# Kernel optimization log

Measured on AMD Instinct MI355X. Metric: run time of the kernel, lower is better.

The kernel has to match this reference:

```python
import jax, jax.numpy as jnp
import numpy as np

B, T, C = 2, 2048, 2048
H, HKV, D = 16, 4, 128
GROUPS = H // HKV  # num_key_value_groups
EPS = 1e-6


def setup_inputs() -> dict:
    key = jax.random.key(0)
    ks = jax.random.split(key, 6)
    s = 0.02
    return {
        "hidden_states": jax.random.normal(ks[0], (B, T, C), jnp.float32),
        "Wq": jax.random.normal(ks[1], (C, H * D), jnp.float32) * s,
        "Wk": jax.random.normal(ks[2], (C, HKV * D), jnp.float32) * s,
        "Wv": jax.random.normal(ks[3], (C, HKV * D), jnp.float32) * s,
        "Wo": jax.random.normal(ks[4], (H * D, C), jnp.float32) * s,
        "keep_mask": jax.random.randint(ks[5], (T,), 0, 2) > 0,
    }


def reference(hidden_states, Wq, Wk, Wv, Wo, keep_mask):
    # Base attention (standard causal GQA attention with output_attentions=True)
    q = (hidden_states @ Wq).reshape(B, T, H, D).transpose(0, 2, 1, 3)      # [B,H,T,D]
    k = (hidden_states @ Wk).reshape(B, T, HKV, D).transpose(0, 2, 1, 3)    # [B,Hkv,S,D]
    v = (hidden_states @ Wv).reshape(B, T, HKV, D).transpose(0, 2, 1, 3)    # [B,Hkv,S,D]
    k_rep = jnp.repeat(k, GROUPS, axis=1)                                    # [B,H,S,D]
    v_rep = jnp.repeat(v, GROUPS, axis=1)                                    # [B,H,S,D]
    scale = 1.0 / jnp.sqrt(jnp.float32(D))
    scores = jnp.einsum("bhtd,bhsd->bhts", q, k_rep) * scale                 # [B,H,T,S]
    causal = jnp.tril(jnp.ones((T, T), dtype=bool))
    scores = jnp.where(causal[None, None], scores, jnp.float32(-1e9))
    attn_w = jax.nn.softmax(scores, axis=-1)                                 # [B,H,T,S]

    # ScratchpadPrunedAttention: mask dropped positions, renormalize,
    # recompute context and o_proj.
    keep = keep_mask.astype(attn_w.dtype)[None, None, None, :]               # [1,1,1,S]
    attn_w = attn_w * keep
    attn_w = attn_w / (attn_w.sum(-1, keepdims=True) + EPS)
    new_ctx = jnp.einsum("bhts,bhsd->bhtd", attn_w, v_rep)                   # [B,H,T,D]
    new_ctx = new_ctx.transpose(0, 2, 1, 3).reshape(B, T, H * D)             # [B,T,H*D]
    out = new_ctx @ Wo                                                        # [B,T,C]
    return out, attn_w
```

## Files before the change

kernel.cpp:

```cpp
#include <hip/hip_runtime.h>
#include <hip/hip_bf16.h>
#include <stdint.h>

#define B_ 2
#define T_ 2048
#define C_ 2048
#define H_ 16
#define HKV_ 4
#define D_ 128
#define M_ (B_*T_)
static constexpr float SCL = 0.08838834764831845f * 1.4426950408889634f;
static constexpr float EPS_ = 1e-6f;

typedef short bf16x8 __attribute__((ext_vector_type(8)));
typedef float f32x4 __attribute__((ext_vector_type(4)));

__device__ __forceinline__ f32x4 zero4() {
  f32x4 v; v[0] = 0.f; v[1] = 0.f; v[2] = 0.f; v[3] = 0.f; return v;
}

__device__ __forceinline__ unsigned short f2bf(float x) {
  union { float f; unsigned u; } v; v.f = x;
  unsigned r = (v.u + 0x7FFFu + ((v.u >> 16) & 1u)) >> 16;
  return (unsigned short)r;
}

__device__ __forceinline__ void gl_lds16(const void* g, void* l) {
  __builtin_amdgcn_global_load_lds((const __attribute__((address_space(1))) void*)g,
                                   (__attribute__((address_space(3))) void*)l, 16, 0, 0);
}

__global__ void k_cvt(const float* __restrict__ in, unsigned short* __restrict__ out, int n) {
  int i = (blockIdx.x * blockDim.x + threadIdx.x) * 8;
  int stride = gridDim.x * blockDim.x * 8;
  for (; i < n; i += stride) {
    float4 a = *(const float4*)(in + i);
    float4 b = *(const float4*)(in + i + 4);
    ushort4 o0; o0.x = f2bf(a.x); o0.y = f2bf(a.y); o0.z = f2bf(a.z); o0.w = f2bf(a.w);
    ushort4 o1; o1.x = f2bf(b.x); o1.y = f2bf(b.y); o1.z = f2bf(b.z); o1.w = f2bf(b.w);
    *(ushort4*)(out + i) = o0;
    *(ushort4*)(out + i + 4) = o1;
  }
}

__global__ void k_cvt_t(const float* __restrict__ in, unsigned short* __restrict__ out,
                        int R, int Cc) {
  __shared__ float ld[32][33];
  int c0 = blockIdx.x * 32, r0 = blockIdx.y * 32;
  int x = threadIdx.x, y = threadIdx.y;
#pragma unroll
  for (int i = 0; i < 4; i++)
    ld[y * 4 + i][x] = in[(size_t)(r0 + y * 4 + i) * Cc + c0 + x];
  __syncthreads();
#pragma unroll
  for (int i = 0; i < 4; i++)
    out[(size_t)(c0 + y * 4 + i) * R + r0 + x] = f2bf(ld[x][y * 4 + i]);
}

template <int WRITE_F32>
__global__ __launch_bounds__(256) void k_gemm(const unsigned short* __restrict__ A,
                                              const unsigned short* __restrict__ Bt,
                                              void* __restrict__ Cout,
                                              int Mdim, int Ndim, int K) {
  __shared__ __align__(16) unsigned short As[128 * 64];
  __shared__ __align__(16) unsigned short Bs[128 * 64];
  const int tid = threadIdx.x;
  const int wid = tid >> 6, lane = tid & 63;
  const int wm = wid >> 1, wn = wid & 1;
  const int m0 = blockIdx.y * 128, n0 = blockIdx.x * 128;
  const int lrow = tid >> 3, lcol = (tid & 7) * 8;
  const int g = lane >> 4, lr = lane & 15;

  f32x4 acc[4][4];
#pragma unroll
  for (int i = 0; i < 4; i++)
#pragma unroll
    for (int j = 0; j < 4; j++) acc[i][j] = zero4();

  for (int k0 = 0; k0 < K; k0 += 64) {
    __syncthreads();
#pragma unroll
    for (int it = 0; it < 4; it++) {
      gl_lds16(A + (size_t)(m0 + lrow + it * 32) * K + k0 + lcol, (void*)(As + tid * 8 + it * 2048));
      gl_lds16(Bt + (size_t)(n0 + lrow + it * 32) * K + k0 + lcol, (void*)(Bs + tid * 8 + it * 2048));
    }
    __syncthreads();
#pragma unroll
    for (int kk = 0; kk < 2; kk++) {
      bf16x8 af[4], bfr[4];
#pragma unroll
      for (int i = 0; i < 4; i++)
        af[i] = *(const bf16x8*)(As + (wm * 64 + i * 16 + lr) * 64 + kk * 32 + g * 8);
#pragma unroll
      for (int j = 0; j < 4; j++)
        bfr[j] = *(const bf16x8*)(Bs + (wn * 64 + j * 16 + lr) * 64 + kk * 32 + g * 8);
#pragma unroll
      for (int i = 0; i < 4; i++)
#pragma unroll
        for (int j = 0; j < 4; j++)
          acc[i][j] = __builtin_amdgcn_mfma_f32_16x16x32_bf16(af[i], bfr[j], acc[i][j], 0, 0, 0);
    }
  }

#pragma unroll
  for (int i = 0; i < 4; i++)
#pragma unroll
    for (int j = 0; j < 4; j++)
#pragma unroll
      for (int r = 0; r < 4; r++) {
        int row = m0 + wm * 64 + i * 16 + g * 4 + r;
        int col = n0 + wn * 64 + j * 16 + lr;
        if (WRITE_F32)
          ((float*)Cout)[(size_t)row * Ndim + col] = acc[i][j][r];
        else
          ((unsigned short*)Cout)[(size_t)row * Ndim + col] = f2bf(acc[i][j][r]);
      }
}

__global__ __launch_bounds__(256) void k_attn(const unsigned short* __restrict__ qb,
                                              const unsigned short* __restrict__ kb,
                                              const unsigned short* __restrict__ vt,
                                              const int* __restrict__ mask,
                                              float* __restrict__ attn,
                                              unsigned short* __restrict__ ctx)
{
  __shared__ __align__(16) unsigned short Ks[64 * 128];
  __shared__ __align__(16) unsigned short Vs[128 * 64];
  __shared__ __align__(16) unsigned short Ps[4][16 * 64];
  __shared__ float keeps[2048];

  const int tid = threadIdx.x;
  const int wid = tid >> 6, lane = tid & 63;
  const int g = lane >> 4, lr = lane & 15;
  const int lr7 = lr & 7;
  const int qt = 31 - blockIdx.y;
  const int bh = blockIdx.x;
  const int b = bh >> 4, h = bh & 15, hkv = h >> 2;
  const int qbase = qt * 64;

  const unsigned short* qp = qb + (size_t)(b * T_ + qbase) * 2048 + h * 128;
  const unsigned short* kp = kb + (size_t)(b * T_) * 512 + hkv * 128;
  const unsigned short* vp = vt + (size_t)(hkv * 128) * 4096 + b * T_;
  float* ap = attn + (size_t)(bh * T_ + qbase) * 2048;
  unsigned short* cp = ctx + (size_t)(b * T_ + qbase) * 2048 + h * 128;

#pragma unroll
  for (int i = 0; i < 8; i++)
    keeps[tid * 8 + i] = (mask[tid * 8 + i] != 0) ? 1.0f : 0.0f;

  bf16x8 qa[4];
#pragma unroll
  for (int ks = 0; ks < 4; ks++)
    qa[ks] = *(const bf16x8*)(qp + (size_t)(wid * 16 + lr) * 2048 + ks * 32 + g * 8);

  const int ntile = qt + 1;
  float z[4] = {0, 0, 0, 0}, zk[4] = {0, 0, 0, 0};

  const int srow = tid >> 4;
  const int scolb = ((tid & 15) * 16) ^ ((srow & 7) << 4);
  const int vrow = tid >> 3;
  const int vcolb = ((tid & 7) * 16) ^ ((vrow & 7) << 4);

  for (int st = 0; st < ntile; st++) {
    int s0 = st * 64;
    __syncthreads();
#pragma unroll
    for (int it = 0; it < 4; it++)
      gl_lds16(kp + (size_t)(s0 + srow + it * 16) * 512 + (scolb >> 1),
               (void*)(Ks + tid * 8 + it * 2048));
    __syncthreads();
#pragma unroll
    for (int j = 0; j < 4; j++) {
      f32x4 sc = zero4();
      const unsigned short* kbase = Ks + (j * 16 + lr) * 128;
#pragma unroll
      for (int ks = 0; ks < 4; ks++) {
        bf16x8 kf = *(const bf16x8*)(kbase + (((ks * 64 + g * 16) ^ (lr7 << 4)) >> 1));
        sc = __builtin_amdgcn_mfma_f32_16x16x32_bf16(qa[ks], kf, sc, 0, 0, 0);
      }
      int sg = s0 + j * 16 + lr;
      float kpv = keeps[sg];
#pragma unroll
      for (int r = 0; r < 4; r++) {
        int tg = qbase + wid * 16 + g * 4 + r;
        float e = (sg <= tg) ? __builtin_amdgcn_exp2f(sc[r] * SCL) : 0.0f;
        z[r] += e;
        zk[r] += e * kpv;
      }
    }
  }
#pragma unroll
  for (int r = 0; r < 4; r++) {
#pragma unroll
    for (int m = 1; m < 16; m <<= 1) {
      z[r] += __shfl_xor(z[r], m);
      zk[r] += __shfl_xor(zk[r], m);
    }
  }
  float inv[4];
#pragma unroll
  for (int r = 0; r < 4; r++) inv[r] = 1.0f / (zk[r] + EPS_ * z[r]);

  f32x4 cacc[8];
#pragma unroll
  for (int n = 0; n < 8; n++) cacc[n] = zero4();

  for (int st = 0; st < 32; st++) {
    int s0 = st * 64;
    if (s0 > qbase + 63) {
      float4 zf; zf.x = 0.f; zf.y = 0.f; zf.z = 0.f; zf.w = 0.f;
#pragma unroll
      for (int it = 0; it < 4; it++) {
        int row = (tid >> 4) + it * 16;
        *(float4*)(ap + (size_t)row * 2048 + s0 + (tid & 15) * 4) = zf;
      }
      continue;
    }
    __syncthreads();
#pragma unroll
    for (int it = 0; it < 4; it++) {
      gl_lds16(kp + (size_t)(s0 + srow + it * 16) * 512 + (scolb >> 1),
               (void*)(Ks + tid * 8 + it * 2048));
      gl_lds16(vp + (size_t)(vrow + it * 32) * 4096 + s0 + (vcolb >> 1),
               (void*)(Vs + tid * 8 + it * 2048));
    }
    __syncthreads();
#pragma unroll
    for (int j = 0; j < 4; j++) {
      f32x4 sc = zero4();
      const unsigned short* kbase = Ks + (j * 16 + lr) * 128;
#pragma unroll
      for (int ks = 0; ks < 4; ks++) {
        bf16x8 kf = *(const bf16x8*)(kbase + (((ks * 64 + g * 16) ^ (lr7 << 4)) >> 1));
        sc = __builtin_amdgcn_mfma_f32_16x16x32_bf16(qa[ks], kf, sc, 0, 0, 0);
      }
      int sg = s0 + j * 16 + lr;
      float kpv = keeps[sg];
#pragma unroll
      for (int r = 0; r < 4; r++) {
        int row = wid * 16 + g * 4 + r;
        int tg = qbase + row;
        float e = (sg <= tg) ? __builtin_amdgcn_exp2f(sc[r] * SCL) : 0.0f;
        float a = e * kpv * inv[r];
        ap[(size_t)row * 2048 + sg] = a;
        int prow = g * 4 + r;
        Ps[wid][prow * 64 + (((j * 32 + lr * 2) ^ ((prow & 7) << 4)) >> 1)] = f2bf(a);
      }
    }
    asm volatile("s_waitcnt lgkmcnt(0)" ::: "memory");
    __builtin_amdgcn_sched_barrier(0);
#pragma unroll
    for (int kk = 0; kk < 2; kk++) {
      bf16x8 pa = *(const bf16x8*)(&Ps[wid][lr * 64 + (((kk * 64 + g * 16) ^ (lr7 << 4)) >> 1)]);
#pragma unroll
      for (int n = 0; n < 8; n++) {
        bf16x8 vf = *(const bf16x8*)(Vs + (n * 16 + lr) * 64 + (((kk * 64 + g * 16) ^ (lr7 << 4)) >> 1));
        cacc[n] = __builtin_amdgcn_mfma_f32_16x16x32_bf16(pa, vf, cacc[n], 0, 0, 0);
      }
    }
  }

#pragma unroll
  for (int n = 0; n < 8; n++)
#pragma unroll
    for (int r = 0; r < 4; r++)
      cp[(size_t)(wid * 16 + g * 4 + r) * 2048 + n * 16 + lr] = f2bf(cacc[n][r]);
}

extern "C" void kernel_launch(void* const* d_in, const int* in_sizes, int n_in,
                              void* d_out, int out_size, void* d_ws, size_t ws_size,
                              hipStream_t stream) {
  const float* hs = (const float*)d_in[0];
  const float* Wq = (const float*)d_in[1];
  const float* Wk = (const float*)d_in[2];
  const float* Wv = (const float*)d_in[3];
  const float* Wo = (const float*)d_in[4];
  const int* mask = (const int*)d_in[5];

  char* w = (char*)d_ws;
  unsigned short* hsb = (unsigned short*)w; w += (size_t)M_ * C_ * 2;
  unsigned short* Wqt = (unsigned short*)w; w += (size_t)2048 * 2048 * 2;
  unsigned short* Wkt = (unsigned short*)w; w += (size_t)512 * 2048 * 2;
  unsigned short* Wvt = (unsigned short*)w; w += (size_t)512 * 2048 * 2;
  unsigned short* Wot = (unsigned short*)w; w += (size_t)2048 * 2048 * 2;
  unsigned short* qbuf = (unsigned short*)w; w += (size_t)M_ * 2048 * 2;
  unsigned short* kbuf = (unsigned short*)w; w += (size_t)M_ * 512 * 2;
  unsigned short* vtb = (unsigned short*)w; w += (size_t)512 * M_ * 2;
  unsigned short* ctxb = (unsigned short*)w; w += (size_t)M_ * 2048 * 2;

  float* out = (float*)d_out;
  float* attn = out + (size_t)M_ * C_;

  k_cvt<<<2048, 256, 0, stream>>>(hs, hsb, M_ * C_);
  k_cvt_t<<<dim3(2048 / 32, 2048 / 32), dim3(32, 8), 0, stream>>>(Wq, Wqt, 2048, 2048);
  k_cvt_t<<<dim3(512 / 32, 2048 / 32), dim3(32, 8), 0, stream>>>(Wk, Wkt, 2048, 512);
  k_cvt_t<<<dim3(512 / 32, 2048 / 32), dim3(32, 8), 0, stream>>>(Wv, Wvt, 2048, 512);
  k_cvt_t<<<dim3(2048 / 32, 2048 / 32), dim3(32, 8), 0, stream>>>(Wo, Wot, 2048, 2048);

  k_gemm<0><<<dim3(2048 / 128, 4096 / 128), 256, 0, stream>>>(hsb, Wqt, qbuf, 4096, 2048, 2048);
  k_gemm<0><<<dim3(512 / 128, 4096 / 128), 256, 0, stream>>>(hsb, Wkt, kbuf, 4096, 512, 2048);
  k_gemm<0><<<dim3(4096 / 128, 512 / 128), 256, 0, stream>>>(Wvt, hsb, vtb, 512, 4096, 2048);

  k_attn<<<dim3(32, 32), 256, 0, stream>>>(qbuf, kbuf, vtb, mask, attn, ctxb);

  k_gemm<1><<<dim3(2048 / 128, 4096 / 128), 256, 0, stream>>>(ctxb, Wot, out, 4096, 2048, 2048);
}
```

Baseline: 429.3 us.

## Enlarge attention tiles to 128 queries, bit-pack mask, swizzle GEMM block order

The attention kernel now uses 512-thread blocks covering 128 query rows, so each K/V tile loaded into shared memory is reused by twice as many queries. The block mapping spreads heads across XCDs, and the second pass walks key tiles in reverse. The keep mask is packed into a bitfield by a new tiny kernel, and zero-filling of the upper attention triangle moves to a single contiguous loop at the end. GEMMs switch to a 1D grid with an XCD-aware swizzle to improve L2 locality. Risks include higher register pressure from launch bounds of 512 threads with 4 blocks, and correctness of the new V swizzle and zero-fill indexing.

```diff
diff --git a/kernel.cpp b/kernel.cpp
--- a/kernel.cpp
+++ b/kernel.cpp
@@ -57,17 +57,30 @@
     out[(size_t)(c0 + y * 4 + i) * R + r0 + x] = f2bf(ld[x][y * 4 + i]);
 }
 
+__global__ void k_maskbits(const int* __restrict__ mask, unsigned int* __restrict__ mb) {
+  int t = threadIdx.x;
+  if (t < 64) {
+    unsigned int w = 0;
+    for (int b = 0; b < 32; b++)
+      if (mask[t * 32 + b] != 0) w |= (1u << b);
+    mb[t] = w;
+  }
+}
+
 template <int WRITE_F32>
 __global__ __launch_bounds__(256) void k_gemm(const unsigned short* __restrict__ A,
                                               const unsigned short* __restrict__ Bt,
                                               void* __restrict__ Cout,
-                                              int Mdim, int Ndim, int K) {
+                                              int Mdim, int Ndim, int K, int nbx) {
   __shared__ __align__(16) unsigned short As[128 * 64];
   __shared__ __align__(16) unsigned short Bs[128 * 64];
   const int tid = threadIdx.x;
   const int wid = tid >> 6, lane = tid & 63;
   const int wm = wid >> 1, wn = wid & 1;
-  const int m0 = blockIdx.y * 128, n0 = blockIdx.x * 128;
+  const int nq = gridDim.x >> 3;
+  const int id = blockIdx.x;
+  const int sw = (id & 7) * nq + (id >> 3);
+  const int m0 = (sw / nbx) * 128, n0 = (sw % nbx) * 128;
   const int lrow = tid >> 3, lcol = (tid & 7) * 8;
   const int g = lane >> 4, lr = lane & 15;
 
@@ -117,26 +130,27 @@
       }
 }
 
-__global__ __launch_bounds__(256) void k_attn(const unsigned short* __restrict__ qb,
-                                              const unsigned short* __restrict__ kb,
-                                              const unsigned short* __restrict__ vt,
-                                              const int* __restrict__ mask,
-                                              float* __restrict__ attn,
-                                              unsigned short* __restrict__ ctx)
+__global__ __launch_bounds__(512, 4) void k_attn(const unsigned short* __restrict__ qb,
+                                                 const unsigned short* __restrict__ kb,
+                                                 const unsigned short* __restrict__ vt,
+                                                 const unsigned int* __restrict__ mb,
+                                                 float* __restrict__ attn,
+                                                 unsigned short* __restrict__ ctx)
 {
   __shared__ __align__(16) unsigned short Ks[64 * 128];
   __shared__ __align__(16) unsigned short Vs[128 * 64];
-  __shared__ __align__(16) unsigned short Ps[4][16 * 64];
-  __shared__ float keeps[2048];
+  __shared__ __align__(16) unsigned short Ps[8][16 * 64];
 
   const int tid = threadIdx.x;
   const int wid = tid >> 6, lane = tid & 63;
   const int g = lane >> 4, lr = lane & 15;
   const int lr7 = lr & 7;
-  const int qt = 31 - blockIdx.y;
-  const int bh = blockIdx.x;
+  const int id = blockIdx.x;
+  const int bh = (id & 7) * 4 + ((id >> 3) & 3);
+  const int qt = 15 - (id >> 5);
   const int b = bh >> 4, h = bh & 15, hkv = h >> 2;
-  const int qbase = qt * 64;
+  const int qbase = qt * 128;
+  const int ntile = 2 * qt + 2;
 
   const unsigned short* qp = qb + (size_t)(b * T_ + qbase) * 2048 + h * 128;
   const unsigned short* kp = kb + (size_t)(b * T_) * 512 + hkv * 128;
@@ -144,30 +158,36 @@
   float* ap = attn + (size_t)(bh * T_ + qbase) * 2048;
   unsigned short* cp = ctx + (size_t)(b * T_ + qbase) * 2048 + h * 128;
 
-#pragma unroll
-  for (int i = 0; i < 8; i++)
-    keeps[tid * 8 + i] = (mask[tid * 8 + i] != 0) ? 1.0f : 0.0f;
-
   bf16x8 qa[4];
 #pragma unroll
   for (int ks = 0; ks < 4; ks++)
     qa[ks] = *(const bf16x8*)(qp + (size_t)(wid * 16 + lr) * 2048 + ks * 32 + g * 8);
-
-  const int ntile = qt + 1;
-  float z[4] = {0, 0, 0, 0}, zk[4] = {0, 0, 0, 0};
 
   const int srow = tid >> 4;
   const int scolb = ((tid & 15) * 16) ^ ((srow & 7) << 4);
   const int vrow = tid >> 3;
   const int vcolb = ((tid & 7) * 16) ^ ((vrow & 7) << 4);
 
+  auto stageK = [&](int st) {
+    const unsigned short* src = kp + (size_t)(st * 64 + srow) * 512 + (scolb >> 1);
+    unsigned short* dst = Ks + tid * 8;
+#pragma unroll
+    for (int it = 0; it < 2; it++)
+      gl_lds16(src + (size_t)it * 32 * 512, (void*)(dst + it * 4096));
+  };
+  auto stageV = [&](int st) {
+    const unsigned short* src = vp + (size_t)vrow * 4096 + st * 64 + (vcolb >> 1);
+    unsigned short* dst = Vs + tid * 8;
+#pragma unroll
+    for (int it = 0; it < 2; it++)
+      gl_lds16(src + (size_t)it * 64 * 4096, (void*)(dst + it * 4096));
+  };
+
+  float z[4] = {0, 0, 0, 0}, zk[4] = {0, 0, 0, 0};
+
   for (int st = 0; st < ntile; st++) {
-    int s0 = st * 64;
-    __syncthreads();
-#pragma unroll
-    for (int it = 0; it < 4; it++)
-      gl_lds16(kp + (size_t)(s0 + srow + it * 16) * 512 + (scolb >> 1),
-               (void*)(Ks + tid * 8 + it * 2048));
+    __syncthreads();
+    stageK(st);
     __syncthreads();
 #pragma unroll
     for (int j = 0; j < 4; j++) {
@@ -178,8 +198,9 @@
         bf16x8 kf = *(const bf16x8*)(kbase + (((ks * 64 + g * 16) ^ (lr7 << 4)) >> 1));
         sc = __builtin_amdgcn_mfma_f32_16x16x32_bf16(qa[ks], kf, sc, 0, 0, 0);
       }
-      int sg = s0 + j * 16 + lr;
-      float kpv = keeps[sg];
+      int sg = st * 64 + j * 16 + lr;
+      unsigned int w = mb[st * 2 + (j >> 1)];
+      float kpv = (float)((w >> ((j & 1) * 16 + lr)) & 1u);
 #pragma unroll
       for (int r = 0; r < 4; r++) {
         int tg = qbase + wid * 16 + g * 4 + r;
@@ -205,26 +226,12 @@
 #pragma unroll
   for (int n = 0; n < 8; n++) cacc[n] = zero4();
 
-  for (int st = 0; st < 32; st++) {
-    int s0 = st * 64;
-    if (s0 > qbase + 63) {
-      float4 zf; zf.x = 0.f; zf.y = 0.f; zf.z = 0.f; zf.w = 0.f;
-#pragma unroll
-      for (int it = 0; it < 4; it++) {
-        int row = (tid >> 4) + it * 16;
-        *(float4*)(ap + (size_t)row * 2048 + s0 + (tid & 15) * 4) = zf;
-      }
-      continue;
-    }
-    __syncthreads();
-#pragma unroll
-    for (int it = 0; it < 4; it++) {
-      gl_lds16(kp + (size_t)(s0 + srow + it * 16) * 512 + (scolb >> 1),
-               (void*)(Ks + tid * 8 + it * 2048));
-      gl_lds16(vp + (size_t)(vrow + it * 32) * 4096 + s0 + (vcolb >> 1),
-               (void*)(Vs + tid * 8 + it * 2048));
-    }
-    __syncthreads();
+  for (int st = ntile - 1; st >= 0; st--) {
+    __syncthreads();
+    stageK(st);
+    stageV(st);
+    __syncthreads();
+    const int s0 = st * 64;
 #pragma unroll
     for (int j = 0; j < 4; j++) {
       f32x4 sc = zero4();
@@ -235,7 +242,8 @@
         sc = __builtin_amdgcn_mfma_f32_16x16x32_bf16(qa[ks], kf, sc, 0, 0, 0);
       }
       int sg = s0 + j * 16 + lr;
-      float kpv = keeps[sg];
+      unsigned int w = mb[st * 2 + (j >> 1)];
+      float kpv = (float)((w >> ((j & 1) * 16 + lr)) & 1u);
 #pragma unroll
       for (int r = 0; r < 4; r++) {
         int row = wid * 16 + g * 4 + r;
@@ -254,7 +262,8 @@
       bf16x8 pa = *(const bf16x8*)(&Ps[wid][lr * 64 + (((kk * 64 + g * 16) ^ (lr7 << 4)) >> 1)]);
 #pragma unroll
       for (int n = 0; n < 8; n++) {
-        bf16x8 vf = *(const bf16x8*)(Vs + (n * 16 + lr) * 64 + (((kk * 64 + g * 16) ^ (lr7 << 4)) >> 1));
+        int vrw = n * 16 + lr;
+        bf16x8 vf = *(const bf16x8*)(Vs + vrw * 64 + (((kk * 64 + g * 16) ^ ((vrw & 7) << 4)) >> 1));
         cacc[n] = __builtin_amdgcn_mfma_f32_16x16x32_bf16(pa, vf, cacc[n], 0, 0, 0);
       }
     }
@@ -265,6 +274,14 @@
 #pragma unroll
     for (int r = 0; r < 4; r++)
       cp[(size_t)(wid * 16 + g * 4 + r) * 2048 + n * 16 + lr] = f2bf(cacc[n][r]);
+
+  const int zc0 = qbase + 128;
+  if (zc0 < 2048) {
+    float4 zf; zf.x = 0.f; zf.y = 0.f; zf.z = 0.f; zf.w = 0.f;
+    float* aprow = ap + (size_t)(tid >> 2) * 2048;
+    for (int c = zc0 + (tid & 3) * 4; c < 2048; c += 16)
+      *(float4*)(aprow + c) = zf;
+  }
 }
 
 extern "C" void kernel_launch(void* const* d_in, const int* in_sizes, int n_in,
@@ -287,6 +304,7 @@
   unsigned short* kbuf = (unsigned short*)w; w += (size_t)M_ * 512 * 2;
   unsigned short* vtb = (unsigned short*)w; w += (size_t)512 * M_ * 2;
   unsigned short* ctxb = (unsigned short*)w; w += (size_t)M_ * 2048 * 2;
+  unsigned int* mbits = (unsigned int*)w;  w += 256;
 
   float* out = (float*)d_out;
   float* attn = out + (size_t)M_ * C_;
@@ -296,12 +314,13 @@
   k_cvt_t<<<dim3(512 / 32, 2048 / 32), dim3(32, 8), 0, stream>>>(Wk, Wkt, 2048, 512);
   k_cvt_t<<<dim3(512 / 32, 2048 / 32), dim3(32, 8), 0, stream>>>(Wv, Wvt, 2048, 512);
   k_cvt_t<<<dim3(2048 / 32, 2048 / 32), dim3(32, 8), 0, stream>>>(Wo, Wot, 2048, 2048);
-
-  k_gemm<0><<<dim3(2048 / 128, 4096 / 128), 256, 0, stream>>>(hsb, Wqt, qbuf, 4096, 2048, 2048);
-  k_gemm<0><<<dim3(512 / 128, 4096 / 128), 256, 0, stream>>>(hsb, Wkt, kbuf, 4096, 512, 2048);
-  k_gemm<0><<<dim3(4096 / 128, 512 / 128), 256, 0, stream>>>(Wvt, hsb, vtb, 512, 4096, 2048);
-
-  k_attn<<<dim3(32, 32), 256, 0, stream>>>(qbuf, kbuf, vtb, mask, attn, ctxb);
-
-  k_gemm<1><<<dim3(2048 / 128, 4096 / 128), 256, 0, stream>>>(ctxb, Wot, out, 4096, 2048, 2048);
-}
+  k_maskbits<<<1, 64, 0, stream>>>(mask, mbits);
+
+  k_gemm<0><<<512, 256, 0, stream>>>(hsb, Wqt, qbuf, 4096, 2048, 2048, 16);
+  k_gemm<0><<<128, 256, 0, stream>>>(hsb, Wkt, kbuf, 4096, 512, 2048, 4);
+  k_gemm<0><<<128, 256, 0, stream>>>(Wvt, hsb, vtb, 512, 4096, 2048, 32);
+
+  k_attn<<<512, 512, 0, stream>>>(qbuf, kbuf, vtb, mbits, attn, ctxb);
+
+  k_gemm<1><<<512, 256, 0, stream>>>(ctxb, Wot, out, 4096, 2048, 2048, 16);
+}
```

Result: slower. 457.5 us (+6.6%).
